# Kernel tuning notes

Measured on AMD Instinct MI355X. Metric: run time of the kernel, lower is better.

## Reference

```python
import jax, jax.numpy as jnp
import numpy as np

N_NODES = 50000
IN_DIM = 128
OUT_DIM = 128
HEADS = 4
HEAD_DIM = OUT_DIM // HEADS
N_EDGES = 800000
LN_EPS = 1e-5
NEG_SLOPE = 0.2


def setup_inputs() -> dict:
    key = jax.random.key(0)
    ks = jax.random.split(key, 8)
    x = jax.random.normal(ks[0], (N_NODES, IN_DIM), dtype=jnp.float32)
    edge_index = jax.random.randint(ks[1], (2, N_EDGES), 0, N_NODES, dtype=jnp.int64)
    s = 1.0 / np.sqrt(IN_DIM)
    W = jax.random.uniform(ks[2], (IN_DIM, HEADS * HEAD_DIM), jnp.float32, -s, s)
    att_src = jax.random.uniform(ks[3], (HEADS, HEAD_DIM), jnp.float32, -s, s)
    att_dst = jax.random.uniform(ks[4], (HEADS, HEAD_DIM), jnp.float32, -s, s)
    bias = jnp.zeros((OUT_DIM,), jnp.float32)
    gamma = jnp.ones((OUT_DIM,), jnp.float32)
    beta = jnp.zeros((OUT_DIM,), jnp.float32)
    return {"x": x, "edge_index": edge_index, "W": W, "att_src": att_src,
            "att_dst": att_dst, "bias": bias, "gamma": gamma, "beta": beta}


def reference(x, edge_index, W, att_src, att_dst, bias, gamma, beta):
    N = x.shape[0]
    H, C = att_src.shape
    # add self-loops (PyG GATConv default)
    loops = jnp.arange(N, dtype=edge_index.dtype)
    src = jnp.concatenate([edge_index[0], loops])  # [E+N]
    dst = jnp.concatenate([edge_index[1], loops])

    h = (x @ W).reshape(N, H, C)                      # [N,H,C]
    a_src = jnp.einsum('nhc,hc->nh', h, att_src)      # [N,H]
    a_dst = jnp.einsum('nhc,hc->nh', h, att_dst)

    e = jax.nn.leaky_relu(a_src[src] + a_dst[dst], NEG_SLOPE)   # [E+N,H]
    emax = jax.ops.segment_max(e, dst, num_segments=N)          # [N,H]
    ex = jnp.exp(e - emax[dst])
    denom = jax.ops.segment_sum(ex, dst, num_segments=N)
    alpha = ex / denom[dst]                                     # [E+N,H]

    msg = h[src] * alpha[:, :, None]                            # [E+N,H,C]
    out = jax.ops.segment_sum(msg, dst, num_segments=N).reshape(N, H * C) + bias

    # LayerNorm
    mu = out.mean(-1, keepdims=True)
    var = ((out - mu) ** 2).mean(-1, keepdims=True)
    hn = (out - mu) / jnp.sqrt(var + LN_EPS) * gamma + beta

    # residual is Identity (in_dim == out_dim); GELU exact; dropout = eval identity
    return jax.nn.gelu(hn + x, approximate=False)
```

## Files before the change

kernel.cpp:

```cpp
#include <hip/hip_runtime.h>
#include <math.h>

#define N_NODES 50000
#define HEADS 4
#define NEG_SLOPE 0.2f
#define LN_EPS 1e-5f
#define SLOTS 80
#define GR 64
#define EPB 2048
#define DSH 8
#define NB 196
#define CAP 40

typedef short short8 __attribute__((ext_vector_type(8)));
typedef float f32x4 __attribute__((ext_vector_type(4)));


__device__ __forceinline__ short f2bf(float f) {
    unsigned u = __float_as_uint(f);
    return (short)((u + 0x7fffu + ((u >> 16) & 1u)) >> 16);
}

__device__ __forceinline__ int detect_is64(const int* __restrict__ ei, int t, int* s_flag) {
    if (t < 64) {
        int nz = (ei[2 * t + 1] != 0) ? 1 : 0;
        unsigned long long b = __ballot(nz);
        if (t == 0) *s_flag = (b == 0ULL) ? 1 : 0;
    }
    __syncthreads();
    return *s_flag;
}

__device__ __forceinline__ float s8f(unsigned u, int p) {
    return (float)((int)(u << (24 - 8 * p)) >> 24);
}

__device__ __forceinline__ float edge_w(float v) {
    v = v > 0.f ? v : NEG_SLOPE * v;
    return __expf(v);
}


__global__ __launch_bounds__(256, 4) void gemm_scatter_kernel(
    const float* __restrict__ x, const float* __restrict__ W,
    const float* __restrict__ att_src, const float* __restrict__ att_dst,
    unsigned* __restrict__ hb, float* __restrict__ rec, float* __restrict__ a_dst,
    const int* __restrict__ ei, int E, int nScatter, int nGemm,
    unsigned* __restrict__ staging, int* __restrict__ scnt) {
    __shared__ __align__(16) char smem[40960];
    const int t = threadIdx.x;
    const int b = (int)blockIdx.x;

    const bool isBin = (b % 3) == 0;
    const int rid = isBin ? (b / 3) : (2 * (b / 3) + (b % 3) - 1);

    if (isBin) {
        if (rid >= nScatter) return;
        int is64 = detect_is64(ei, t, (int*)smem);
        int* lcnt = (int*)smem + 64;
        unsigned* cells = (unsigned*)(smem + 1056);
        for (int i = t; i < NB; i += 256) lcnt[i] = 0;
        __syncthreads();

        const int e0 = rid * EPB + t * 8;
        int ss[8], dd[8];
        if (e0 + 8 <= E) {
            if (is64) {
                const uint4* ps4 = (const uint4*)(ei + 2 * (size_t)e0);
                const uint4* pd4 = (const uint4*)(ei + 2 * ((size_t)E + e0));
#pragma unroll
                for (int u = 0; u < 4; ++u) {
                    uint4 qs = ps4[u], qd = pd4[u];
                    ss[2 * u] = (int)qs.x; ss[2 * u + 1] = (int)qs.z;
                    dd[2 * u] = (int)qd.x; dd[2 * u + 1] = (int)qd.z;
                }
            } else {
                const uint4* ps4 = (const uint4*)(ei + e0);
                const uint4* pd4 = (const uint4*)(ei + (size_t)E + e0);
#pragma unroll
                for (int u = 0; u < 2; ++u) {
                    uint4 qs = ps4[u], qd = pd4[u];
                    ss[4 * u] = (int)qs.x; ss[4 * u + 1] = (int)qs.y;
                    ss[4 * u + 2] = (int)qs.z; ss[4 * u + 3] = (int)qs.w;
                    dd[4 * u] = (int)qd.x; dd[4 * u + 1] = (int)qd.y;
                    dd[4 * u + 2] = (int)qd.z; dd[4 * u + 3] = (int)qd.w;
                }
            }
        } else {
#pragma unroll
            for (int u = 0; u < 8; ++u) {
                int e = e0 + u;
                if (e < E) {
                    if (is64) { ss[u] = ei[2 * e]; dd[u] = ei[2 * (E + e)]; }
                    else      { ss[u] = ei[e];     dd[u] = ei[E + e]; }
                } else { ss[u] = -1; dd[u] = 0; }
            }
        }
#pragma unroll
        for (int u = 0; u < 8; ++u) {
            if (ss[u] < 0) continue;
            int bkt = dd[u] >> DSH;
            int p = atomicAdd(&lcnt[bkt], 1);
            if (p < CAP)
                cells[bkt * CAP + p] = (unsigned)ss[u] | ((unsigned)dd[u] << 16);
        }
        __syncthreads();
        uint4* dst4 = (uint4*)(staging + (size_t)rid * NB * CAP);
        const uint4* src4 = (const uint4*)cells;
        for (int i = t; i < NB * CAP / 4; i += 256) dst4[i] = src4[i];
        for (int i = t; i < NB; i += 256)
            scnt[(size_t)rid * NB + i] = min(lcnt[i], CAP);
        return;
    }

    if (rid >= nGemm) return;
    const int rowBase = rid * GR;
    const int l = t & 63;
    const int wv = t >> 6;

    {
        const int nlo = l & 7, khi = l >> 3;
        for (int i = 0; i < 8; ++i) {
            int tile = wv + 4 * i;
            int n = (tile & 15) * 8 + nlo;
            int k8 = (tile >> 4) * 8 + khi;
            short8 pk;
#pragma unroll
            for (int jj = 0; jj < 8; ++jj)
                pk[jj] = f2bf(W[(k8 * 8 + jj) * 128 + n]);
            int us = (k8 & 8) | ((k8 & 7) ^ (n & 7));
            *(short8*)(smem + n * 256 + us * 16) = pk;
        }
    }
    __syncthreads();

    const int g = l >> 4;
    const int c = l & 15;

    f32x4 acc[8];
#pragma unroll
    for (int ct = 0; ct < 8; ++ct) acc[ct] = {0.f, 0.f, 0.f, 0.f};

    {
        int arow = rowBase + wv * 16 + c;
        if (arow >= N_NODES) arow = N_NODES - 1;
        const float* xrow = x + (size_t)arow * 128;
#pragma unroll
        for (int kk = 0; kk < 4; ++kk) {
            float4 xa = *(const float4*)(xrow + kk * 32 + g * 8);
            float4 xb = *(const float4*)(xrow + kk * 32 + g * 8 + 4);
            short8 af;
            af[0] = f2bf(xa.x); af[1] = f2bf(xa.y); af[2] = f2bf(xa.z); af[3] = f2bf(xa.w);
            af[4] = f2bf(xb.x); af[5] = f2bf(xb.y); af[6] = f2bf(xb.z); af[7] = f2bf(xb.w);
#pragma unroll
            for (int ct = 0; ct < 8; ++ct) {
                int n = ct * 16 + c;
                int u = kk * 4 + g;
                int us = (u & 8) | ((u & 7) ^ (n & 7));
                short8 bf = *(const short8*)(smem + n * 256 + us * 16);
                acc[ct] = __builtin_amdgcn_mfma_f32_16x16x32_bf16(af, bf, acc[ct], 0, 0, 0);
            }
        }
    }

    char* ep = smem + 32768 + wv * 2048;
    float asA[4], asB[4], adA[4], adB[4];
#pragma unroll
    for (int h = 0; h < 4; ++h) {
        asA[h] = att_src[h * 32 + c];
        asB[h] = att_src[h * 32 + 16 + c];
        adA[h] = att_dst[h * 32 + c];
        adB[h] = att_dst[h * 32 + 16 + c];
    }
#pragma unroll
    for (int r = 0; r < 4; ++r) {
        float v[8];
#pragma unroll
        for (int ct = 0; ct < 8; ++ct) v[ct] = acc[ct][r];

        float m = fabsf(v[0]);
#pragma unroll
        for (int ct = 1; ct < 8; ++ct) m = fmaxf(m, fabsf(v[ct]));
#pragma unroll
        for (int o = 1; o < 16; o <<= 1) m = fmaxf(m, __shfl_xor(m, o, 64));
        m = fmaxf(m, 1e-20f);
        const float inv = 127.0f / m;

        float sp[4], dp[4];
#pragma unroll
        for (int h = 0; h < 4; ++h) {
            sp[h] = v[2 * h] * asA[h] + v[2 * h + 1] * asB[h];
            dp[h] = v[2 * h] * adA[h] + v[2 * h + 1] * adB[h];
        }
#pragma unroll
        for (int o = 1; o < 16; o <<= 1) {
#pragma unroll
            for (int h = 0; h < 4; ++h) {
                sp[h] += __shfl_xor(sp[h], o, 64);
                dp[h] += __shfl_xor(dp[h], o, 64);
            }
        }
        const int row_l = g * 4 + r;
        const int row = rowBase + wv * 16 + row_l;
        if (c == 0 && row < N_NODES) {
            const float hs = m * (1.0f / 127.0f);
            float4* rw = (float4*)(rec + (size_t)row * 8);
            rw[0] = make_float4(sp[0], hs, sp[1], hs);
            rw[1] = make_float4(sp[2], hs, sp[3], hs);
            a_dst[row * 4 + 0] = dp[0]; a_dst[row * 4 + 1] = dp[1];
            a_dst[row * 4 + 2] = dp[2]; a_dst[row * 4 + 3] = dp[3];
        }
#pragma unroll
        for (int ct = 0; ct < 8; ++ct) {
            int q = __float2int_rn(v[ct] * inv);
            ep[row_l * 128 + ct * 16 + c] = (char)q;
        }
    }

#pragma unroll
    for (int w8 = 0; w8 < 8; ++w8) {
        int idx = w8 * 64 + l;
        int row_l = idx >> 5, tx = idx & 31;
        unsigned word = *(const unsigned*)(ep + row_l * 128 + tx * 4);
        int row = rowBase + wv * 16 + row_l;
        if (row < N_NODES) hb[(size_t)row * 32 + tx] = word;
    }
}

__global__ __launch_bounds__(256) void build_kernel(
    const unsigned* __restrict__ staging, const int* __restrict__ scnt,
    int nScatter, int* __restrict__ cnt, unsigned short* __restrict__ esrc) {
    __shared__ int lcnt2[256];
    const int B = blockIdx.x;
    const int t = threadIdx.x;
    lcnt2[t] = 0;
    __syncthreads();

    for (int blk = t; blk < nScatter; blk += 256) {
        const int c = scnt[(size_t)blk * NB + B];
        const unsigned* cell = staging + ((size_t)blk * NB + B) * CAP;
        for (int j = 0; j < c; j += 4) {
            uint4 q = *(const uint4*)(cell + j);
            const int m = c - j;
            {
                int d = (int)(q.x >> 16);
                int p = atomicAdd(&lcnt2[d & 255], 1);
                if (p < SLOTS) esrc[(size_t)d * SLOTS + p] = (unsigned short)(q.x & 0xffffu);
            }
            if (m > 1) {
                int d = (int)(q.y >> 16);
                int p = atomicAdd(&lcnt2[d & 255], 1);
                if (p < SLOTS) esrc[(size_t)d * SLOTS + p] = (unsigned short)(q.y & 0xffffu);
            }
            if (m > 2) {
                int d = (int)(q.z >> 16);
                int p = atomicAdd(&lcnt2[d & 255], 1);
                if (p < SLOTS) esrc[(size_t)d * SLOTS + p] = (unsigned short)(q.z & 0xffffu);
            }
            if (m > 3) {
                int d = (int)(q.w >> 16);
                int p = atomicAdd(&lcnt2[d & 255], 1);
                if (p < SLOTS) esrc[(size_t)d * SLOTS + p] = (unsigned short)(q.w & 0xffffu);
            }
        }
    }
    __syncthreads();
    const int d = (B << DSH) + t;
    if (d < N_NODES) cnt[d] = lcnt2[t];
}

__global__ __launch_bounds__(256) void gat_fused_kernel(
    const int* __restrict__ cnt, const unsigned short* __restrict__ esrc,
    const float* __restrict__ rec, const float* __restrict__ a_dst,
    const unsigned* __restrict__ hb,
    const float* __restrict__ bias, const float* __restrict__ x,
    const float* __restrict__ gamma, const float* __restrict__ beta,
    float* __restrict__ out) {
    const int t = threadIdx.x;
    const int l = t & 63;
    const int wv = t >> 6;
    const int g = l >> 4;
    const int j = l & 15;
    const int n = blockIdx.x * 16 + wv * 4 + g;
    const int hh = j >> 2;

    const uint2* hb2 = (const uint2*)hb;
    const uint2* rec2 = (const uint2*)rec;

    const float adst_me = a_dst[(n << 2) + hh];
    uint2 rS = rec2[(unsigned)(n * 4 + hh)];
    float ps = edge_w(__uint_as_float(rS.x) + adst_me);

    uint2 hvS = hb2[(unsigned)(n * 16 + j)];
    {
        const float uS = ps * __uint_as_float(rS.y);
        float acc0 = uS * s8f(hvS.x, 0), acc1 = uS * s8f(hvS.x, 1);
        float acc2 = uS * s8f(hvS.x, 2), acc3 = uS * s8f(hvS.x, 3);
        float acc4 = uS * s8f(hvS.y, 0), acc5 = uS * s8f(hvS.y, 1);
        float acc6 = uS * s8f(hvS.y, 2), acc7 = uS * s8f(hvS.y, 3);

        const int deg = min(cnt[n], SLOTS);
        const unsigned short* row = esrc + n * SLOTS;

        for (int base = 0; base < deg; base += 8) {
            const int rem = deg - base;
            uint4 q = *(const uint4*)(row + base);
            int s0 = (int)(q.x & 0xffffu);
            int s1 = (rem > 1) ? (int)(q.x >> 16) : n;
            int s2 = (rem > 2) ? (int)(q.y & 0xffffu) : n;
            int s3 = (rem > 3) ? (int)(q.y >> 16) : n;
            int s4 = (rem > 4) ? (int)(q.z & 0xffffu) : n;
            int s5 = (rem > 5) ? (int)(q.z >> 16) : n;
            int s6 = (rem > 6) ? (int)(q.w & 0xffffu) : n;
            int s7 = (rem > 7) ? (int)(q.w >> 16) : n;

            uint2 r0 = rec2[(unsigned)(s0 * 4 + hh)];
            uint2 r1 = rec2[(unsigned)(s1 * 4 + hh)];
            uint2 r2 = rec2[(unsigned)(s2 * 4 + hh)];
            uint2 r3 = rec2[(unsigned)(s3 * 4 + hh)];
            uint2 r4 = rec2[(unsigned)(s4 * 4 + hh)];
            uint2 r5 = rec2[(unsigned)(s5 * 4 + hh)];
            uint2 r6 = rec2[(unsigned)(s6 * 4 + hh)];
            uint2 r7 = rec2[(unsigned)(s7 * 4 + hh)];
            uint2 h0 = hb2[(unsigned)(s0 * 16 + j)];
            uint2 h1 = hb2[(unsigned)(s1 * 16 + j)];
            uint2 h2 = hb2[(unsigned)(s2 * 16 + j)];
            uint2 h3 = hb2[(unsigned)(s3 * 16 + j)];
            uint2 h4 = hb2[(unsigned)(s4 * 16 + j)];
            uint2 h5 = hb2[(unsigned)(s5 * 16 + j)];
            uint2 h6 = hb2[(unsigned)(s6 * 16 + j)];
            uint2 h7 = hb2[(unsigned)(s7 * 16 + j)];

            float w0 = edge_w(__uint_as_float(r0.x) + adst_me);
            float w1 = (rem > 1) ? edge_w(__uint_as_float(r1.x) + adst_me) : 0.f;
            float w2 = (rem > 2) ? edge_w(__uint_as_float(r2.x) + adst_me) : 0.f;
            float w3 = (rem > 3) ? edge_w(__uint_as_float(r3.x) + adst_me) : 0.f;
            float w4 = (rem > 4) ? edge_w(__uint_as_float(r4.x) + adst_me) : 0.f;
            float w5 = (rem > 5) ? edge_w(__uint_as_float(r5.x) + adst_me) : 0.f;
            float w6 = (rem > 6) ? edge_w(__uint_as_float(r6.x) + adst_me) : 0.f;
            float w7 = (rem > 7) ? edge_w(__uint_as_float(r7.x) + adst_me) : 0.f;
            ps += (w0 + w1 + w2 + w3) + (w4 + w5 + w6 + w7);

            float u0 = w0 * __uint_as_float(r0.y), u1 = w1 * __uint_as_float(r1.y);
            float u2 = w2 * __uint_as_float(r2.y), u3 = w3 * __uint_as_float(r3.y);
            float u4 = w4 * __uint_as_float(r4.y), u5 = w5 * __uint_as_float(r5.y);
            float u6 = w6 * __uint_as_float(r6.y), u7 = w7 * __uint_as_float(r7.y);

            acc0 += u0 * s8f(h0.x, 0) + u1 * s8f(h1.x, 0) + u2 * s8f(h2.x, 0) + u3 * s8f(h3.x, 0)
                  + u4 * s8f(h4.x, 0) + u5 * s8f(h5.x, 0) + u6 * s8f(h6.x, 0) + u7 * s8f(h7.x, 0);
            acc1 += u0 * s8f(h0.x, 1) + u1 * s8f(h1.x, 1) + u2 * s8f(h2.x, 1) + u3 * s8f(h3.x, 1)
                  + u4 * s8f(h4.x, 1) + u5 * s8f(h5.x, 1) + u6 * s8f(h6.x, 1) + u7 * s8f(h7.x, 1);
            acc2 += u0 * s8f(h0.x, 2) + u1 * s8f(h1.x, 2) + u2 * s8f(h2.x, 2) + u3 * s8f(h3.x, 2)
                  + u4 * s8f(h4.x, 2) + u5 * s8f(h5.x, 2) + u6 * s8f(h6.x, 2) + u7 * s8f(h7.x, 2);
            acc3 += u0 * s8f(h0.x, 3) + u1 * s8f(h1.x, 3) + u2 * s8f(h2.x, 3) + u3 * s8f(h3.x, 3)
                  + u4 * s8f(h4.x, 3) + u5 * s8f(h5.x, 3) + u6 * s8f(h6.x, 3) + u7 * s8f(h7.x, 3);
            acc4 += u0 * s8f(h0.y, 0) + u1 * s8f(h1.y, 0) + u2 * s8f(h2.y, 0) + u3 * s8f(h3.y, 0)
                  + u4 * s8f(h4.y, 0) + u5 * s8f(h5.y, 0) + u6 * s8f(h6.y, 0) + u7 * s8f(h7.y, 0);
            acc5 += u0 * s8f(h0.y, 1) + u1 * s8f(h1.y, 1) + u2 * s8f(h2.y, 1) + u3 * s8f(h3.y, 1)
                  + u4 * s8f(h4.y, 1) + u5 * s8f(h5.y, 1) + u6 * s8f(h6.y, 1) + u7 * s8f(h7.y, 1);
            acc6 += u0 * s8f(h0.y, 2) + u1 * s8f(h1.y, 2) + u2 * s8f(h2.y, 2) + u3 * s8f(h3.y, 2)
                  + u4 * s8f(h4.y, 2) + u5 * s8f(h5.y, 2) + u6 * s8f(h6.y, 2) + u7 * s8f(h7.y, 2);
            acc7 += u0 * s8f(h0.y, 3) + u1 * s8f(h1.y, 3) + u2 * s8f(h2.y, 3) + u3 * s8f(h3.y, 3)
                  + u4 * s8f(h4.y, 3) + u5 * s8f(h5.y, 3) + u6 * s8f(h6.y, 3) + u7 * s8f(h7.y, 3);
        }

        const float inv = 1.0f / ps;
        const float4* bias4 = (const float4*)bias;
        float4 bA = bias4[j * 2], bB = bias4[j * 2 + 1];
        float v0 = acc0 * inv + bA.x, v1 = acc1 * inv + bA.y;
        float v2 = acc2 * inv + bA.z, v3 = acc3 * inv + bA.w;
        float v4 = acc4 * inv + bB.x, v5 = acc5 * inv + bB.y;
        float v6 = acc6 * inv + bB.z, v7 = acc7 * inv + bB.w;

        float s1 = v0 + v1 + v2 + v3 + v4 + v5 + v6 + v7;
        float s2 = v0 * v0 + v1 * v1 + v2 * v2 + v3 * v3 +
                   v4 * v4 + v5 * v5 + v6 * v6 + v7 * v7;
#pragma unroll
        for (int o = 1; o < 16; o <<= 1) {
            s1 += __shfl_xor(s1, o, 64);
            s2 += __shfl_xor(s2, o, 64);
        }
        float mu = s1 * (1.0f / 128.0f);
        float var = s2 * (1.0f / 128.0f) - mu * mu;
        float rstd = rsqrtf(var + LN_EPS);

        const float4* gamma4 = (const float4*)gamma;
        const float4* beta4 = (const float4*)beta;
        const float4* x4 = (const float4*)x;
        float4 gA = gamma4[j * 2], gB = gamma4[j * 2 + 1];
        float4 eA = beta4[j * 2], eB = beta4[j * 2 + 1];
        float4 xA = x4[(size_t)n * 32 + j * 2], xB = x4[(size_t)n * 32 + j * 2 + 1];

        float r0f = (v0 - mu) * rstd * gA.x + eA.x + xA.x;
        float r1f = (v1 - mu) * rstd * gA.y + eA.y + xA.y;
        float r2f = (v2 - mu) * rstd * gA.z + eA.z + xA.z;
        float r3f = (v3 - mu) * rstd * gA.w + eA.w + xA.w;
        float r4f = (v4 - mu) * rstd * gB.x + eB.x + xB.x;
        float r5f = (v5 - mu) * rstd * gB.y + eB.y + xB.y;
        float r6f = (v6 - mu) * rstd * gB.z + eB.z + xB.z;
        float r7f = (v7 - mu) * rstd * gB.w + eB.w + xB.w;

        const float k = 0.70710678118654752440f;
        float4 oA = make_float4(0.5f * r0f * (1.0f + erff(r0f * k)),
                                0.5f * r1f * (1.0f + erff(r1f * k)),
                                0.5f * r2f * (1.0f + erff(r2f * k)),
                                0.5f * r3f * (1.0f + erff(r3f * k)));
        float4 oB = make_float4(0.5f * r4f * (1.0f + erff(r4f * k)),
                                0.5f * r5f * (1.0f + erff(r5f * k)),
                                0.5f * r6f * (1.0f + erff(r6f * k)),
                                0.5f * r7f * (1.0f + erff(r7f * k)));
        float4* out4 = (float4*)out;
        out4[(size_t)n * 32 + j * 2] = oA;
        out4[(size_t)n * 32 + j * 2 + 1] = oB;
    }
}


extern "C" void kernel_launch(void* const* d_in, const int* in_sizes, int n_in,
                              void* d_out, int out_size, void* d_ws, size_t ws_size,
                              hipStream_t stream) {
    const float* x       = (const float*)d_in[0];
    const int*   ei      = (const int*)d_in[1];
    const float* W       = (const float*)d_in[2];
    const float* att_src = (const float*)d_in[3];
    const float* att_dst = (const float*)d_in[4];
    const float* bias    = (const float*)d_in[5];
    const float* gamma   = (const float*)d_in[6];
    const float* beta    = (const float*)d_in[7];
    float* out = (float*)d_out;
    const int E = in_sizes[1] / 2;

    unsigned* hb         = (unsigned*)d_ws;
    float* rec           = (float*)(hb + (size_t)N_NODES * 32);
    float* a_dst         = rec + (size_t)N_NODES * 8;
    int*   cnt           = (int*)(a_dst + N_NODES * 4);
    unsigned short* esrc = (unsigned short*)(cnt + N_NODES);

    const int nScatter = (E + EPB - 1) / EPB;
    unsigned* staging    = (unsigned*)(esrc + (size_t)N_NODES * SLOTS);
    int* scnt            = (int*)(staging + (size_t)nScatter * NB * CAP);

    const int nGemm = (N_NODES + GR - 1) / GR;
    int total = 3 * nScatter;
    const int needGemm = 3 * ((nGemm + 1) / 2);
    if (needGemm > total) total = needGemm;

    gemm_scatter_kernel<<<total, 256, 0, stream>>>(
        x, W, att_src, att_dst, hb, rec, a_dst, ei, E, nScatter, nGemm,
        staging, scnt);
    build_kernel<<<NB, 256, 0, stream>>>(staging, scnt, nScatter, cnt, esrc);
    gat_fused_kernel<<<N_NODES / 16, 256, 0, stream>>>(cnt, esrc, rec, a_dst, hb,
                                                       bias, x, gamma, beta, out);
}
```

Measured before the change: 145.5 us.

## Fuse adjacency build into aggregation kernel and use offset uint8 features

The separate build kernel and the global esrc/cnt arrays are removed. Each aggregation block now scans the staging cells of its 256-node bucket and keeps, in shared memory, only the edges whose destination lies in its own 16 nodes. This saves one launch plus the global write and re-read of the neighbour lists. The cost is that every bucket's staging data is read redundantly by 16 blocks. Separately, features are stored as int8 values offset by 128, so they can be unpacked with a cheaper unsigned byte-to-float conversion, and a running sum of weights subtracts the offset afterwards.

```diff
diff --git a/kernel.cpp b/kernel.cpp
--- a/kernel.cpp
+++ b/kernel.cpp
@@ -31,8 +31,8 @@
     return *s_flag;
 }
 
-__device__ __forceinline__ float s8f(unsigned u, int p) {
-    return (float)((int)(u << (24 - 8 * p)) >> 24);
+__device__ __forceinline__ float u8f(unsigned u, int p) {
+    return (float)((u >> (8 * p)) & 0xffu);
 }
 
 __device__ __forceinline__ float edge_w(float v) {
@@ -213,7 +213,7 @@
 #pragma unroll
         for (int ct = 0; ct < 8; ++ct) {
             int q = __float2int_rn(v[ct] * inv);
-            ep[row_l * 128 + ct * 16 + c] = (char)q;
+            ep[row_l * 128 + ct * 16 + c] = (char)(q + 128);
         }
     }
 
@@ -227,13 +227,21 @@
     }
 }
 
-__global__ __launch_bounds__(256) void build_kernel(
-    const unsigned* __restrict__ staging, const int* __restrict__ scnt,
-    int nScatter, int* __restrict__ cnt, unsigned short* __restrict__ esrc) {
-    __shared__ int lcnt2[256];
-    const int B = blockIdx.x;
+__global__ __launch_bounds__(256) void gat_fused_kernel(
+    const unsigned* __restrict__ staging, const int* __restrict__ scnt, int nScatter,
+    const float* __restrict__ rec, const float* __restrict__ a_dst,
+    const unsigned* __restrict__ hb,
+    const float* __restrict__ bias, const float* __restrict__ x,
+    const float* __restrict__ gamma, const float* __restrict__ beta,
+    float* __restrict__ out) {
+    __shared__ __align__(16) unsigned short lists[16 * SLOTS];
+    __shared__ int lcnt[16];
     const int t = threadIdx.x;
-    lcnt2[t] = 0;
+    const int n0 = blockIdx.x * 16;
+    const int B = n0 >> DSH;
+    const int grp16 = n0 >> 4;
+
+    if (t < 16) lcnt[t] = 0;
     __syncthreads();
 
     for (int blk = t; blk < nScatter; blk += 256) {
@@ -244,44 +252,42 @@
             const int m = c - j;
             {
                 int d = (int)(q.x >> 16);
-                int p = atomicAdd(&lcnt2[d & 255], 1);
-                if (p < SLOTS) esrc[(size_t)d * SLOTS + p] = (unsigned short)(q.x & 0xffffu);
+                if ((d >> 4) == grp16) {
+                    int p = atomicAdd(&lcnt[d & 15], 1);
+                    if (p < SLOTS) lists[(d & 15) * SLOTS + p] = (unsigned short)(q.x & 0xffffu);
+                }
             }
             if (m > 1) {
                 int d = (int)(q.y >> 16);
-                int p = atomicAdd(&lcnt2[d & 255], 1);
-                if (p < SLOTS) esrc[(size_t)d * SLOTS + p] = (unsigned short)(q.y & 0xffffu);
+                if ((d >> 4) == grp16) {
+                    int p = atomicAdd(&lcnt[d & 15], 1);
+                    if (p < SLOTS) lists[(d & 15) * SLOTS + p] = (unsigned short)(q.y & 0xffffu);
+                }
             }
             if (m > 2) {
                 int d = (int)(q.z >> 16);
-                int p = atomicAdd(&lcnt2[d & 255], 1);
-                if (p < SLOTS) esrc[(size_t)d * SLOTS + p] = (unsigned short)(q.z & 0xffffu);
+                if ((d >> 4) == grp16) {
+                    int p = atomicAdd(&lcnt[d & 15], 1);
+                    if (p < SLOTS) lists[(d & 15) * SLOTS + p] = (unsigned short)(q.z & 0xffffu);
+                }
             }
             if (m > 3) {
                 int d = (int)(q.w >> 16);
-                int p = atomicAdd(&lcnt2[d & 255], 1);
-                if (p < SLOTS) esrc[(size_t)d * SLOTS + p] = (unsigned short)(q.w & 0xffffu);
+                if ((d >> 4) == grp16) {
+                    int p = atomicAdd(&lcnt[d & 15], 1);
+                    if (p < SLOTS) lists[(d & 15) * SLOTS + p] = (unsigned short)(q.w & 0xffffu);
+                }
             }
         }
     }
     __syncthreads();
-    const int d = (B << DSH) + t;
-    if (d < N_NODES) cnt[d] = lcnt2[t];
-}
-
-__global__ __launch_bounds__(256) void gat_fused_kernel(
-    const int* __restrict__ cnt, const unsigned short* __restrict__ esrc,
-    const float* __restrict__ rec, const float* __restrict__ a_dst,
-    const unsigned* __restrict__ hb,
-    const float* __restrict__ bias, const float* __restrict__ x,
-    const float* __restrict__ gamma, const float* __restrict__ beta,
-    float* __restrict__ out) {
-    const int t = threadIdx.x;
+
     const int l = t & 63;
     const int wv = t >> 6;
     const int g = l >> 4;
     const int j = l & 15;
-    const int n = blockIdx.x * 16 + wv * 4 + g;
+    const int li = wv * 4 + g;
+    const int n = n0 + li;
     const int hh = j >> 2;
 
     const uint2* hb2 = (const uint2*)hb;
@@ -294,13 +300,14 @@
     uint2 hvS = hb2[(unsigned)(n * 16 + j)];
     {
         const float uS = ps * __uint_as_float(rS.y);
-        float acc0 = uS * s8f(hvS.x, 0), acc1 = uS * s8f(hvS.x, 1);
-        float acc2 = uS * s8f(hvS.x, 2), acc3 = uS * s8f(hvS.x, 3);
-        float acc4 = uS * s8f(hvS.y, 0), acc5 = uS * s8f(hvS.y, 1);
-        float acc6 = uS * s8f(hvS.y, 2), acc7 = uS * s8f(hvS.y, 3);
-
-        const int deg = min(cnt[n], SLOTS);
-        const unsigned short* row = esrc + n * SLOTS;
+        float su = uS;
+        float acc0 = uS * u8f(hvS.x, 0), acc1 = uS * u8f(hvS.x, 1);
+        float acc2 = uS * u8f(hvS.x, 2), acc3 = uS * u8f(hvS.x, 3);
+        float acc4 = uS * u8f(hvS.y, 0), acc5 = uS * u8f(hvS.y, 1);
+        float acc6 = uS * u8f(hvS.y, 2), acc7 = uS * u8f(hvS.y, 3);
+
+        const int deg = min(lcnt[li], SLOTS);
+        const unsigned short* row = lists + li * SLOTS;
 
         for (int base = 0; base < deg; base += 8) {
             const int rem = deg - base;
@@ -345,32 +352,34 @@
             float u2 = w2 * __uint_as_float(r2.y), u3 = w3 * __uint_as_float(r3.y);
             float u4 = w4 * __uint_as_float(r4.y), u5 = w5 * __uint_as_float(r5.y);
             float u6 = w6 * __uint_as_float(r6.y), u7 = w7 * __uint_as_float(r7.y);
-
-            acc0 += u0 * s8f(h0.x, 0) + u1 * s8f(h1.x, 0) + u2 * s8f(h2.x, 0) + u3 * s8f(h3.x, 0)
-                  + u4 * s8f(h4.x, 0) + u5 * s8f(h5.x, 0) + u6 * s8f(h6.x, 0) + u7 * s8f(h7.x, 0);
-            acc1 += u0 * s8f(h0.x, 1) + u1 * s8f(h1.x, 1) + u2 * s8f(h2.x, 1) + u3 * s8f(h3.x, 1)
-                  + u4 * s8f(h4.x, 1) + u5 * s8f(h5.x, 1) + u6 * s8f(h6.x, 1) + u7 * s8f(h7.x, 1);
-            acc2 += u0 * s8f(h0.x, 2) + u1 * s8f(h1.x, 2) + u2 * s8f(h2.x, 2) + u3 * s8f(h3.x, 2)
-                  + u4 * s8f(h4.x, 2) + u5 * s8f(h5.x, 2) + u6 * s8f(h6.x, 2) + u7 * s8f(h7.x, 2);
-            acc3 += u0 * s8f(h0.x, 3) + u1 * s8f(h1.x, 3) + u2 * s8f(h2.x, 3) + u3 * s8f(h3.x, 3)
-                  + u4 * s8f(h4.x, 3) + u5 * s8f(h5.x, 3) + u6 * s8f(h6.x, 3) + u7 * s8f(h7.x, 3);
-            acc4 += u0 * s8f(h0.y, 0) + u1 * s8f(h1.y, 0) + u2 * s8f(h2.y, 0) + u3 * s8f(h3.y, 0)
-                  + u4 * s8f(h4.y, 0) + u5 * s8f(h5.y, 0) + u6 * s8f(h6.y, 0) + u7 * s8f(h7.y, 0);
-            acc5 += u0 * s8f(h0.y, 1) + u1 * s8f(h1.y, 1) + u2 * s8f(h2.y, 1) + u3 * s8f(h3.y, 1)
-                  + u4 * s8f(h4.y, 1) + u5 * s8f(h5.y, 1) + u6 * s8f(h6.y, 1) + u7 * s8f(h7.y, 1);
-            acc6 += u0 * s8f(h0.y, 2) + u1 * s8f(h1.y, 2) + u2 * s8f(h2.y, 2) + u3 * s8f(h3.y, 2)
-                  + u4 * s8f(h4.y, 2) + u5 * s8f(h5.y, 2) + u6 * s8f(h6.y, 2) + u7 * s8f(h7.y, 2);
-            acc7 += u0 * s8f(h0.y, 3) + u1 * s8f(h1.y, 3) + u2 * s8f(h2.y, 3) + u3 * s8f(h3.y, 3)
-                  + u4 * s8f(h4.y, 3) + u5 * s8f(h5.y, 3) + u6 * s8f(h6.y, 3) + u7 * s8f(h7.y, 3);
+            su += (u0 + u1 + u2 + u3) + (u4 + u5 + u6 + u7);
+
+            acc0 += u0 * u8f(h0.x, 0) + u1 * u8f(h1.x, 0) + u2 * u8f(h2.x, 0) + u3 * u8f(h3.x, 0)
+                  + u4 * u8f(h4.x, 0) + u5 * u8f(h5.x, 0) + u6 * u8f(h6.x, 0) + u7 * u8f(h7.x, 0);
+            acc1 += u0 * u8f(h0.x, 1) + u1 * u8f(h1.x, 1) + u2 * u8f(h2.x, 1) + u3 * u8f(h3.x, 1)
+                  + u4 * u8f(h4.x, 1) + u5 * u8f(h5.x, 1) + u6 * u8f(h6.x, 1) + u7 * u8f(h7.x, 1);
+            acc2 += u0 * u8f(h0.x, 2) + u1 * u8f(h1.x, 2) + u2 * u8f(h2.x, 2) + u3 * u8f(h3.x, 2)
+                  + u4 * u8f(h4.x, 2) + u5 * u8f(h5.x, 2) + u6 * u8f(h6.x, 2) + u7 * u8f(h7.x, 2);
+            acc3 += u0 * u8f(h0.x, 3) + u1 * u8f(h1.x, 3) + u2 * u8f(h2.x, 3) + u3 * u8f(h3.x, 3)
+                  + u4 * u8f(h4.x, 3) + u5 * u8f(h5.x, 3) + u6 * u8f(h6.x, 3) + u7 * u8f(h7.x, 3);
+            acc4 += u0 * u8f(h0.y, 0) + u1 * u8f(h1.y, 0) + u2 * u8f(h2.y, 0) + u3 * u8f(h3.y, 0)
+                  + u4 * u8f(h4.y, 0) + u5 * u8f(h5.y, 0) + u6 * u8f(h6.y, 0) + u7 * u8f(h7.y, 0);
+            acc5 += u0 * u8f(h0.y, 1) + u1 * u8f(h1.y, 1) + u2 * u8f(h2.y, 1) + u3 * u8f(h3.y, 1)
+                  + u4 * u8f(h4.y, 1) + u5 * u8f(h5.y, 1) + u6 * u8f(h6.y, 1) + u7 * u8f(h7.y, 1);
+            acc6 += u0 * u8f(h0.y, 2) + u1 * u8f(h1.y, 2) + u2 * u8f(h2.y, 2) + u3 * u8f(h3.y, 2)
+                  + u4 * u8f(h4.y, 2) + u5 * u8f(h5.y, 2) + u6 * u8f(h6.y, 2) + u7 * u8f(h7.y, 2);
+            acc7 += u0 * u8f(h0.y, 3) + u1 * u8f(h1.y, 3) + u2 * u8f(h2.y, 3) + u3 * u8f(h3.y, 3)
+                  + u4 * u8f(h4.y, 3) + u5 * u8f(h5.y, 3) + u6 * u8f(h6.y, 3) + u7 * u8f(h7.y, 3);
         }
 
         const float inv = 1.0f / ps;
+        const float cs = 128.0f * su;
         const float4* bias4 = (const float4*)bias;
         float4 bA = bias4[j * 2], bB = bias4[j * 2 + 1];
-        float v0 = acc0 * inv + bA.x, v1 = acc1 * inv + bA.y;
-        float v2 = acc2 * inv + bA.z, v3 = acc3 * inv + bA.w;
-        float v4 = acc4 * inv + bB.x, v5 = acc5 * inv + bB.y;
-        float v6 = acc6 * inv + bB.z, v7 = acc7 * inv + bB.w;
+        float v0 = (acc0 - cs) * inv + bA.x, v1 = (acc1 - cs) * inv + bA.y;
+        float v2 = (acc2 - cs) * inv + bA.z, v3 = (acc3 - cs) * inv + bA.w;
+        float v4 = (acc4 - cs) * inv + bB.x, v5 = (acc5 - cs) * inv + bB.y;
+        float v6 = (acc6 - cs) * inv + bB.z, v7 = (acc7 - cs) * inv + bB.w;
 
         float s1 = v0 + v1 + v2 + v3 + v4 + v5 + v6 + v7;
         float s2 = v0 * v0 + v1 * v1 + v2 * v2 + v3 * v3 +
@@ -433,11 +442,9 @@
     unsigned* hb         = (unsigned*)d_ws;
     float* rec           = (float*)(hb + (size_t)N_NODES * 32);
     float* a_dst         = rec + (size_t)N_NODES * 8;
-    int*   cnt           = (int*)(a_dst + N_NODES * 4);
-    unsigned short* esrc = (unsigned short*)(cnt + N_NODES);
 
     const int nScatter = (E + EPB - 1) / EPB;
-    unsigned* staging    = (unsigned*)(esrc + (size_t)N_NODES * SLOTS);
+    unsigned* staging    = (unsigned*)(a_dst + (size_t)N_NODES * 4);
     int* scnt            = (int*)(staging + (size_t)nScatter * NB * CAP);
 
     const int nGemm = (N_NODES + GR - 1) / GR;
@@ -448,7 +455,7 @@
     gemm_scatter_kernel<<<total, 256, 0, stream>>>(
         x, W, att_src, att_dst, hb, rec, a_dst, ei, E, nScatter, nGemm,
         staging, scnt);
-    build_kernel<<<NB, 256, 0, stream>>>(staging, scnt, nScatter, cnt, esrc);
-    gat_fused_kernel<<<N_NODES / 16, 256, 0, stream>>>(cnt, esrc, rec, a_dst, hb,
+    gat_fused_kernel<<<N_NODES / 16, 256, 0, stream>>>(staging, scnt, nScatter,
+                                                       rec, a_dst, hb,
                                                        bias, x, gamma, beta, out);
 }
```

Result: slower. 160.9 us (+10.5%).
